# Optimization experiments

Hardware: AMD Instinct MI355X
Metric: run time of the kernel (lower is better)

## Reference

```python
import jax, jax.numpy as jnp
import numpy as np

N = 100000  # nodes
E = 1600000  # edges
F = 128      # features
C = 16       # classes
K = 2        # propagation hops


def setup_inputs() -> dict:
    key = jax.random.key(0)
    k1, k2, k3 = jax.random.split(key, 3)
    x = jax.random.normal(k1, (N, F), dtype=jnp.float32)
    edge_index = jax.random.randint(k2, (2, E), 0, N, dtype=jnp.int64)
    W = jax.random.normal(k3, (F, C), dtype=jnp.float32) * (1.0 / np.sqrt(F))
    b = jnp.zeros((C,), dtype=jnp.float32)
    return {"x": x, "edge_index": edge_index, "W": W, "b": b}


def _sg_propagate(x, row, col, num_nodes):
    # GCN symmetric normalization with self-loops already appended to row/col.
    ones = jnp.ones(row.shape, dtype=x.dtype)
    deg = jax.ops.segment_sum(ones, row, num_segments=num_nodes)
    dinv = jnp.where(deg > 0, jax.lax.rsqrt(deg), jnp.zeros_like(deg))
    norm = dinv[row] * dinv[col]  # [E+N]
    for _ in range(K):
        # gather messages from source nodes, scale, scatter-sum to destinations
        x = jax.ops.segment_sum(norm[:, None] * x[col], row, num_segments=num_nodes)
    return x


def reference(x, edge_index, W, b):
    num_nodes = x.shape[0]
    loops = jnp.arange(num_nodes, dtype=edge_index.dtype)
    row = jnp.concatenate([edge_index[0], loops])
    col = jnp.concatenate([edge_index[1], loops])
    h = _sg_propagate(x, row, col, num_nodes)  # [N, F]
    logits = h @ W + b                          # [N, C]
    return jax.nn.log_softmax(logits, axis=1)
```

## Files before the change

### kernel.cpp

```cpp
#include <hip/hip_runtime.h>
#include <hip/hip_fp16.h>
#include <math.h>

#define NN 100000
#define NE 1600000
#define NF 128
#define NC 16
#define NBUK 391
#define BSH 8
#define BNODES 256
#define CHUNK 8192
#define P1B 196
#define CMASK 0x1FFFF
#define MAXEDG 4800

__global__ void k_init(int* __restrict__ bcur) {
    int n = threadIdx.x;
    if (n < NBUK) bcur[n] = n * MAXEDG;
}

__global__ __launch_bounds__(512) void k_part(const int* __restrict__ row,
                                              const int* __restrict__ col,
                                              int* __restrict__ bcur,
                                              int* __restrict__ pairs) {
    __shared__ int hist[NBUK];
    __shared__ int loff[NBUK];
    __shared__ int gbase[NBUK];
    __shared__ int stage[CHUNK];
    __shared__ unsigned short bkt[CHUNK];
    const int t = threadIdx.x;
    const int cb = blockIdx.x * CHUNK;
    const int ccnt = min(CHUNK, NE - cb);
    const int nquad = ccnt >> 2;
    for (int i = t; i < NBUK; i += 512) hist[i] = 0;
    __syncthreads();

    int rr[16], cc[16], rk[16];
    #pragma unroll
    for (int j = 0; j < 4; ++j) {
        int q = j * 512 + t;
        if (q < nquad) {
            int4 r4 = *(const int4*)&row[cb + 4 * q];
            int4 c4 = *(const int4*)&col[cb + 4 * q];
            rr[4 * j] = r4.x; rr[4 * j + 1] = r4.y; rr[4 * j + 2] = r4.z; rr[4 * j + 3] = r4.w;
            cc[4 * j] = c4.x; cc[4 * j + 1] = c4.y; cc[4 * j + 2] = c4.z; cc[4 * j + 3] = c4.w;
            #pragma unroll
            for (int k = 0; k < 4; ++k)
                rk[4 * j + k] = atomicAdd(&hist[rr[4 * j + k] >> BSH], 1);
        }
    }
    __syncthreads();
    if (t < 64) {
        int loc[7];
        int acc = 0;
        #pragma unroll
        for (int j = 0; j < 7; ++j) {
            int idx = t * 7 + j;
            int v = (idx < NBUK) ? hist[idx] : 0;
            loc[j] = acc;
            acc += v;
        }
        int s = acc;
        #pragma unroll
        for (int o = 1; o < 64; o <<= 1) {
            int u = __shfl_up(s, o, 64);
            if (t >= o) s += u;
        }
        int excl = s - acc;
        #pragma unroll
        for (int j = 0; j < 7; ++j) {
            int idx = t * 7 + j;
            if (idx < NBUK) loff[idx] = excl + loc[j];
        }
    }
    __syncthreads();
    for (int i = t; i < NBUK; i += 512)
        if (hist[i] > 0) gbase[i] = atomicAdd(&bcur[i], hist[i]);
    __syncthreads();
    #pragma unroll
    for (int j = 0; j < 4; ++j) {
        int q = j * 512 + t;
        if (q < nquad) {
            #pragma unroll
            for (int k = 0; k < 4; ++k) {
                int r = rr[4 * j + k];
                int b = r >> BSH;
                int pos = loff[b] + rk[4 * j + k];
                stage[pos] = ((r & (BNODES - 1)) << 17) | cc[4 * j + k];
                bkt[pos] = (unsigned short)b;
            }
        }
    }
    __syncthreads();
    for (int s = t; s < ccnt; s += 512) {
        int b = bkt[s];
        pairs[gbase[b] + (s - loff[b])] = stage[s];
    }
}

__global__ __launch_bounds__(256) void k_fine(const int* __restrict__ bcur,
                                              const int* __restrict__ pairs,
                                              int2* __restrict__ rpc,
                                              float* __restrict__ dinv,
                                              int* __restrict__ csr) {
    __shared__ int h[BNODES];
    __shared__ int hs[BNODES];
    const int b = blockIdx.x;
    const int nb = b << BSH;
    const int t = threadIdx.x;
    h[t] = 0;
    __syncthreads();
    const int st = b * MAXEDG;
    const int m = bcur[b] - st;
    for (int i = t; i < m; i += 256)
        atomicAdd(&h[__builtin_nontemporal_load(&pairs[st + i]) >> 17], 1);
    __syncthreads();
    int v = h[t];
    hs[t] = v;
    __syncthreads();
    for (int o = 1; o < 256; o <<= 1) {
        int a = (t >= o) ? hs[t - o] : 0;
        __syncthreads();
        hs[t] += a;
        __syncthreads();
    }
    int excl = hs[t] - v;
    int n0 = nb + t;
    if (n0 < NN) {
        rpc[n0] = make_int2(st + excl, v);
        dinv[n0] = rsqrtf((float)(v + 1));
    }
    __syncthreads();
    h[t] = excl;
    __syncthreads();
    for (int i = t; i < m; i += 256) {
        int pk = __builtin_nontemporal_load(&pairs[st + i]);
        int pos = atomicAdd(&h[pk >> 17], 1);
        csr[st + pos] = pk & CMASK;
    }
}

#define GEMM_ROWS 64
#define XPAD (NF + 4)

__global__ __launch_bounds__(256) void k_gemm(const float* __restrict__ x,
                                              const float* __restrict__ W,
                                              const float* __restrict__ dinv,
                                              __half* __restrict__ u) {
    __shared__ float Wl[NF * NC];
    __shared__ float xs[GEMM_ROWS * XPAD];
    const int t = threadIdx.x;
    for (int i = t; i < NF * NC; i += 256) Wl[i] = W[i];
    const int rbase = blockIdx.x * GEMM_ROWS;
    const float4* x4 = (const float4*)x;
    for (int i = t; i < GEMM_ROWS * (NF / 4); i += 256) {
        int lrow = i >> 5, k4 = i & 31;
        int r = rbase + lrow;
        float4 v = (r < NN) ? x4[(size_t)r * (NF / 4) + k4]
                            : make_float4(0.f, 0.f, 0.f, 0.f);
        *(float4*)&xs[lrow * XPAD + 4 * k4] = v;
    }
    __syncthreads();
    const int lr = t >> 2;
    const int cg = t & 3;
    float4 acc = make_float4(0.f, 0.f, 0.f, 0.f);
    #pragma unroll
    for (int k4 = 0; k4 < NF / 4; ++k4) {
        float4 xv = *(const float4*)&xs[lr * XPAD + 4 * k4];
        float4 w0 = *(const float4*)&Wl[(4 * k4 + 0) * NC + cg * 4];
        float4 w1 = *(const float4*)&Wl[(4 * k4 + 1) * NC + cg * 4];
        float4 w2 = *(const float4*)&Wl[(4 * k4 + 2) * NC + cg * 4];
        float4 w3 = *(const float4*)&Wl[(4 * k4 + 3) * NC + cg * 4];
        acc.x = fmaf(xv.x, w0.x, fmaf(xv.y, w1.x, fmaf(xv.z, w2.x, fmaf(xv.w, w3.x, acc.x))));
        acc.y = fmaf(xv.x, w0.y, fmaf(xv.y, w1.y, fmaf(xv.z, w2.y, fmaf(xv.w, w3.y, acc.y))));
        acc.z = fmaf(xv.x, w0.z, fmaf(xv.y, w1.z, fmaf(xv.z, w2.z, fmaf(xv.w, w3.z, acc.z))));
        acc.w = fmaf(xv.x, w0.w, fmaf(xv.y, w1.w, fmaf(xv.z, w2.w, fmaf(xv.w, w3.w, acc.w))));
    }
    int r = rbase + lr;
    if (r < NN) {
        float d = dinv[r];
        __half2 h0 = __floats2half2_rn(acc.x * d, acc.y * d);
        __half2 h1 = __floats2half2_rn(acc.z * d, acc.w * d);
        float2 o;
        o.x = *(float*)&h0;
        o.y = *(float*)&h1;
        ((float2*)u)[((size_t)r << 2) + cg] = o;
    }
}


__device__ __forceinline__ void acc16(float4 rw, float* a) {
    float2 f0 = __half22float2(*(__half2*)&rw.x);
    float2 f1 = __half22float2(*(__half2*)&rw.y);
    float2 f2 = __half22float2(*(__half2*)&rw.z);
    float2 f3 = __half22float2(*(__half2*)&rw.w);
    a[0] += f0.x; a[1] += f0.y; a[2] += f1.x; a[3] += f1.y;
    a[4] += f2.x; a[5] += f2.y; a[6] += f3.x; a[7] += f3.y;
}

__global__ __launch_bounds__(256) void k_hop1(const int2* __restrict__ rpc,
                                              const float* __restrict__ dinv,
                                              const int* __restrict__ csr,
                                              const float4* __restrict__ u,
                                              float4* __restrict__ u1) {
    int t = blockIdx.x * 256 + threadIdx.x;
    if (t >= NN * 2) return;
    int n = t >> 1, half = t & 1;
    int2 rc = rpc[n];
    int s = rc.x, m = rc.y;
    float a[8] = {0.f, 0.f, 0.f, 0.f, 0.f, 0.f, 0.f, 0.f};
    acc16(u[(n << 1) + half], a);
    int i = 0;
    for (; i + 8 <= m; i += 8) {
        int cc[8];
        #pragma unroll
        for (int j = 0; j < 8; ++j) cc[j] = __builtin_nontemporal_load(&csr[s + i + j]);
        #pragma unroll
        for (int j = 0; j < 8; ++j) acc16(u[(cc[j] << 1) + half], a);
    }
    for (; i < m; ++i)
        acc16(u[(__builtin_nontemporal_load(&csr[s + i]) << 1) + half], a);
    float d = dinv[n];
    float sc = d * d;
    __half2 h0 = __floats2half2_rn(a[0] * sc, a[1] * sc);
    __half2 h1 = __floats2half2_rn(a[2] * sc, a[3] * sc);
    __half2 h2 = __floats2half2_rn(a[4] * sc, a[5] * sc);
    __half2 h3 = __floats2half2_rn(a[6] * sc, a[7] * sc);
    float4 o;
    o.x = *(float*)&h0; o.y = *(float*)&h1;
    o.z = *(float*)&h2; o.w = *(float*)&h3;
    u1[t] = o;
}

__global__ __launch_bounds__(256) void k_hop2(const int2* __restrict__ rpc,
                                              const float* __restrict__ dinv,
                                              const int* __restrict__ csr,
                                              const float4* __restrict__ u1,
                                              const float* __restrict__ bias,
                                              float* __restrict__ out) {
    int t = blockIdx.x * 256 + threadIdx.x;
    if (t >= NN * 2) return;
    int n = t >> 1, half = t & 1;
    int2 rc = rpc[n];
    int s = rc.x, m = rc.y;
    float a[8] = {0.f, 0.f, 0.f, 0.f, 0.f, 0.f, 0.f, 0.f};
    acc16(u1[(n << 1) + half], a);
    int i = 0;
    for (; i + 8 <= m; i += 8) {
        int cc[8];
        #pragma unroll
        for (int j = 0; j < 8; ++j) cc[j] = __builtin_nontemporal_load(&csr[s + i + j]);
        #pragma unroll
        for (int j = 0; j < 8; ++j) acc16(u1[(cc[j] << 1) + half], a);
    }
    for (; i < m; ++i)
        acc16(u1[(__builtin_nontemporal_load(&csr[s + i]) << 1) + half], a);
    float d = dinv[n];
    float v[8];
    const float4* b4 = (const float4*)bias;
    float4 bv0 = b4[half * 2], bv1 = b4[half * 2 + 1];
    v[0] = fmaf(d, a[0], bv0.x); v[1] = fmaf(d, a[1], bv0.y);
    v[2] = fmaf(d, a[2], bv0.z); v[3] = fmaf(d, a[3], bv0.w);
    v[4] = fmaf(d, a[4], bv1.x); v[5] = fmaf(d, a[5], bv1.y);
    v[6] = fmaf(d, a[6], bv1.z); v[7] = fmaf(d, a[7], bv1.w);
    float mx = v[0];
    #pragma unroll
    for (int j = 1; j < 8; ++j) mx = fmaxf(mx, v[j]);
    mx = fmaxf(mx, __shfl_xor(mx, 1, 2));
    float sm = 0.f;
    #pragma unroll
    for (int j = 0; j < 8; ++j) sm += expf(v[j] - mx);
    sm += __shfl_xor(sm, 1, 2);
    float lse = mx + logf(sm);
    float4* o4 = (float4*)out;
    float4 o0, o1;
    o0.x = v[0] - lse; o0.y = v[1] - lse; o0.z = v[2] - lse; o0.w = v[3] - lse;
    o1.x = v[4] - lse; o1.y = v[5] - lse; o1.z = v[6] - lse; o1.w = v[7] - lse;
    o4[((size_t)n << 2) + half * 2]     = o0;
    o4[((size_t)n << 2) + half * 2 + 1] = o1;
}

extern "C" void kernel_launch(void* const* d_in, const int* in_sizes, int n_in,
                              void* d_out, int out_size, void* d_ws, size_t ws_size,
                              hipStream_t stream) {
    const float* x    = (const float*)d_in[0];
    const int*   ei   = (const int*)d_in[1];
    const float* W    = (const float*)d_in[2];
    const float* bias = (const float*)d_in[3];
    float* out = (float*)d_out;

    const int* row = ei;
    const int* col = ei + NE;

    char* ws = (char*)d_ws;
    size_t off = 0;
    auto carve = [&](size_t bytes) -> void* {
        void* p = ws + off;
        off += (bytes + 255) & ~(size_t)255;
        return p;
    };
    int2*   rpc   = (int2*)  carve((size_t)NN * sizeof(int2));
    float*  dinv  = (float*) carve((size_t)NN * sizeof(float));
    int*    bcur  = (int*)   carve((size_t)NBUK * sizeof(int));
    int*    pairs = (int*)   carve((size_t)NBUK * MAXEDG * sizeof(int));
    int*    csr   = (int*)   carve((size_t)NBUK * MAXEDG * sizeof(int));
    float4* u     = (float4*)carve((size_t)NN * NC * sizeof(__half));
    float4* u1    = (float4*)carve((size_t)NN * NC * sizeof(__half));

    k_init<<<1, 512, 0, stream>>>(bcur);
    k_part<<<P1B, 512, 0, stream>>>(row, col, bcur, pairs);
    k_fine<<<NBUK, 256, 0, stream>>>(bcur, pairs, rpc, dinv, csr);

    k_gemm<<<(NN + GEMM_ROWS - 1) / GEMM_ROWS, 256, 0, stream>>>(x, W, dinv, (__half*)u);

    const int HB = (NN * 2 + 255) / 256;
    k_hop1<<<HB, 256, 0, stream>>>(rpc, dinv, csr, u, u1);
    k_hop2<<<HB, 256, 0, stream>>>(rpc, dinv, csr, u1, bias, out);
}
```

Baseline: 101.5 us.

## Pad CSR rows to multiples of four and sort nodes by degree per bucket

Each node's CSR segment is padded to a multiple of four entries, filled with a dummy node index that points at a zeroed row in u and u1. This lets the hop kernels read neighbour indices as int4 vectors without a tail loop. Within each 256-node bucket, nodes are reordered by degree so that lanes in a wavefront have similar trip counts, which cuts divergence. Input loads also switch to nontemporal. The cost is a larger CSR buffer, extra padding writes, an indirection through the node order, and scattered output writes.

New measurement: 117.7 us. +16.0%, slower.

```diff
diff --git a/kernel.cpp b/kernel.cpp
--- a/kernel.cpp
+++ b/kernel.cpp
@@ -13,6 +13,10 @@
 #define P1B 196
 #define CMASK 0x1FFFF
 #define MAXEDG 4800
+#define CSRS 5632
+
+typedef int   iv4 __attribute__((ext_vector_type(4)));
+typedef float fv4 __attribute__((ext_vector_type(4)));
 
 __global__ void k_init(int* __restrict__ bcur) {
     int n = threadIdx.x;
@@ -35,13 +39,15 @@
     for (int i = t; i < NBUK; i += 512) hist[i] = 0;
     __syncthreads();
 
+    const iv4* row4 = (const iv4*)row;
+    const iv4* col4 = (const iv4*)col;
     int rr[16], cc[16], rk[16];
     #pragma unroll
     for (int j = 0; j < 4; ++j) {
         int q = j * 512 + t;
         if (q < nquad) {
-            int4 r4 = *(const int4*)&row[cb + 4 * q];
-            int4 c4 = *(const int4*)&col[cb + 4 * q];
+            iv4 r4 = __builtin_nontemporal_load(row4 + (cb >> 2) + q);
+            iv4 c4 = __builtin_nontemporal_load(col4 + (cb >> 2) + q);
             rr[4 * j] = r4.x; rr[4 * j + 1] = r4.y; rr[4 * j + 2] = r4.z; rr[4 * j + 3] = r4.w;
             cc[4 * j] = c4.x; cc[4 * j + 1] = c4.y; cc[4 * j + 2] = c4.z; cc[4 * j + 3] = c4.w;
             #pragma unroll
@@ -102,13 +108,16 @@
                                               const int* __restrict__ pairs,
                                               int2* __restrict__ rpc,
                                               float* __restrict__ dinv,
-                                              int* __restrict__ csr) {
+                                              int* __restrict__ csr,
+                                              int* __restrict__ norder) {
     __shared__ int h[BNODES];
     __shared__ int hs[BNODES];
+    __shared__ int dh[64];
     const int b = blockIdx.x;
     const int nb = b << BSH;
     const int t = threadIdx.x;
     h[t] = 0;
+    if (t < 64) dh[t] = 0;
     __syncthreads();
     const int st = b * MAXEDG;
     const int m = bcur[b] - st;
@@ -116,7 +125,8 @@
         atomicAdd(&h[__builtin_nontemporal_load(&pairs[st + i]) >> 17], 1);
     __syncthreads();
     int v = h[t];
-    hs[t] = v;
+    int pd = (v + 3) & ~3;
+    hs[t] = pd;
     __syncthreads();
     for (int o = 1; o < 256; o <<= 1) {
         int a = (t >= o) ? hs[t - o] : 0;
@@ -124,20 +134,33 @@
         hs[t] += a;
         __syncthreads();
     }
-    int excl = hs[t] - v;
+    int base = b * CSRS + hs[t] - pd;
     int n0 = nb + t;
     if (n0 < NN) {
-        rpc[n0] = make_int2(st + excl, v);
+        rpc[n0] = make_int2(base, v);
         dinv[n0] = rsqrtf((float)(v + 1));
     }
-    __syncthreads();
-    h[t] = excl;
-    __syncthreads();
+    int dcl = min(v, 63);
+    int drank = atomicAdd(&dh[dcl], 1);
+    h[t] = base;
+    __syncthreads();
+    if (t < 64) {
+        int val = dh[t], s = val;
+        #pragma unroll
+        for (int o = 1; o < 64; o <<= 1) {
+            int u = __shfl_up(s, o, 64);
+            if (t >= o) s += u;
+        }
+        dh[t] = s - val;
+    }
+    __syncthreads();
+    norder[nb + dh[dcl] + drank] = n0;
     for (int i = t; i < m; i += 256) {
         int pk = __builtin_nontemporal_load(&pairs[st + i]);
         int pos = atomicAdd(&h[pk >> 17], 1);
-        csr[st + pos] = pk & CMASK;
-    }
+        csr[pos] = pk & CMASK;
+    }
+    for (int j = v; j < pd; ++j) csr[base + j] = NN;
 }
 
 #define GEMM_ROWS 64
@@ -146,18 +169,22 @@
 __global__ __launch_bounds__(256) void k_gemm(const float* __restrict__ x,
                                               const float* __restrict__ W,
                                               const float* __restrict__ dinv,
-                                              __half* __restrict__ u) {
+                                              __half* __restrict__ u,
+                                              __half* __restrict__ u1) {
     __shared__ float Wl[NF * NC];
     __shared__ float xs[GEMM_ROWS * XPAD];
     const int t = threadIdx.x;
     for (int i = t; i < NF * NC; i += 256) Wl[i] = W[i];
     const int rbase = blockIdx.x * GEMM_ROWS;
-    const float4* x4 = (const float4*)x;
+    const fv4* x4 = (const fv4*)x;
     for (int i = t; i < GEMM_ROWS * (NF / 4); i += 256) {
         int lrow = i >> 5, k4 = i & 31;
         int r = rbase + lrow;
-        float4 v = (r < NN) ? x4[(size_t)r * (NF / 4) + k4]
-                            : make_float4(0.f, 0.f, 0.f, 0.f);
+        float4 v = make_float4(0.f, 0.f, 0.f, 0.f);
+        if (r < NN) {
+            fv4 xv = __builtin_nontemporal_load(x4 + (size_t)r * (NF / 4) + k4);
+            v = make_float4(xv.x, xv.y, xv.z, xv.w);
+        }
         *(float4*)&xs[lrow * XPAD + 4 * k4] = v;
     }
     __syncthreads();
@@ -185,6 +212,10 @@
         o.x = *(float*)&h0;
         o.y = *(float*)&h1;
         ((float2*)u)[((size_t)r << 2) + cg] = o;
+    } else if (r == NN) {
+        float2 z = make_float2(0.f, 0.f);
+        ((float2*)u)[((size_t)r << 2) + cg] = z;
+        ((float2*)u1)[((size_t)r << 2) + cg] = z;
     }
 }
 
@@ -198,29 +229,30 @@
     a[4] += f2.x; a[5] += f2.y; a[6] += f3.x; a[7] += f3.y;
 }
 
-__global__ __launch_bounds__(256) void k_hop1(const int2* __restrict__ rpc,
+__global__ __launch_bounds__(256) void k_hop1(const int* __restrict__ norder,
+                                              const int2* __restrict__ rpc,
                                               const float* __restrict__ dinv,
                                               const int* __restrict__ csr,
                                               const float4* __restrict__ u,
                                               float4* __restrict__ u1) {
     int t = blockIdx.x * 256 + threadIdx.x;
-    if (t >= NN * 2) return;
-    int n = t >> 1, half = t & 1;
-    int2 rc = rpc[n];
-    int s = rc.x, m = rc.y;
+    int rank = t >> 1, half = t & 1;
+    int node = norder[rank];
+    if (node >= NN) return;
+    int2 rc = rpc[node];
+    int s4 = rc.x >> 2;
+    int trips = (rc.y + 3) >> 2;
     float a[8] = {0.f, 0.f, 0.f, 0.f, 0.f, 0.f, 0.f, 0.f};
-    acc16(u[(n << 1) + half], a);
-    int i = 0;
-    for (; i + 8 <= m; i += 8) {
-        int cc[8];
-        #pragma unroll
-        for (int j = 0; j < 8; ++j) cc[j] = __builtin_nontemporal_load(&csr[s + i + j]);
-        #pragma unroll
-        for (int j = 0; j < 8; ++j) acc16(u[(cc[j] << 1) + half], a);
-    }
-    for (; i < m; ++i)
-        acc16(u[(__builtin_nontemporal_load(&csr[s + i]) << 1) + half], a);
-    float d = dinv[n];
+    acc16(u[(node << 1) + half], a);
+    const iv4* csr4 = (const iv4*)csr;
+    for (int i = 0; i < trips; ++i) {
+        iv4 c = __builtin_nontemporal_load(csr4 + s4 + i);
+        acc16(u[(c.x << 1) + half], a);
+        acc16(u[(c.y << 1) + half], a);
+        acc16(u[(c.z << 1) + half], a);
+        acc16(u[(c.w << 1) + half], a);
+    }
+    float d = dinv[node];
     float sc = d * d;
     __half2 h0 = __floats2half2_rn(a[0] * sc, a[1] * sc);
     __half2 h1 = __floats2half2_rn(a[2] * sc, a[3] * sc);
@@ -229,33 +261,34 @@
     float4 o;
     o.x = *(float*)&h0; o.y = *(float*)&h1;
     o.z = *(float*)&h2; o.w = *(float*)&h3;
-    u1[t] = o;
-}
-
-__global__ __launch_bounds__(256) void k_hop2(const int2* __restrict__ rpc,
+    u1[(node << 1) + half] = o;
+}
+
+__global__ __launch_bounds__(256) void k_hop2(const int* __restrict__ norder,
+                                              const int2* __restrict__ rpc,
                                               const float* __restrict__ dinv,
                                               const int* __restrict__ csr,
                                               const float4* __restrict__ u1,
                                               const float* __restrict__ bias,
                                               float* __restrict__ out) {
     int t = blockIdx.x * 256 + threadIdx.x;
-    if (t >= NN * 2) return;
-    int n = t >> 1, half = t & 1;
-    int2 rc = rpc[n];
-    int s = rc.x, m = rc.y;
+    int rank = t >> 1, half = t & 1;
+    int node = norder[rank];
+    if (node >= NN) return;
+    int2 rc = rpc[node];
+    int s4 = rc.x >> 2;
+    int trips = (rc.y + 3) >> 2;
     float a[8] = {0.f, 0.f, 0.f, 0.f, 0.f, 0.f, 0.f, 0.f};
-    acc16(u1[(n << 1) + half], a);
-    int i = 0;
-    for (; i + 8 <= m; i += 8) {
-        int cc[8];
-        #pragma unroll
-        for (int j = 0; j < 8; ++j) cc[j] = __builtin_nontemporal_load(&csr[s + i + j]);
-        #pragma unroll
-        for (int j = 0; j < 8; ++j) acc16(u1[(cc[j] << 1) + half], a);
-    }
-    for (; i < m; ++i)
-        acc16(u1[(__builtin_nontemporal_load(&csr[s + i]) << 1) + half], a);
-    float d = dinv[n];
+    acc16(u1[(node << 1) + half], a);
+    const iv4* csr4 = (const iv4*)csr;
+    for (int i = 0; i < trips; ++i) {
+        iv4 c = __builtin_nontemporal_load(csr4 + s4 + i);
+        acc16(u1[(c.x << 1) + half], a);
+        acc16(u1[(c.y << 1) + half], a);
+        acc16(u1[(c.z << 1) + half], a);
+        acc16(u1[(c.w << 1) + half], a);
+    }
+    float d = dinv[node];
     float v[8];
     const float4* b4 = (const float4*)bias;
     float4 bv0 = b4[half * 2], bv1 = b4[half * 2 + 1];
@@ -276,8 +309,8 @@
     float4 o0, o1;
     o0.x = v[0] - lse; o0.y = v[1] - lse; o0.z = v[2] - lse; o0.w = v[3] - lse;
     o1.x = v[4] - lse; o1.y = v[5] - lse; o1.z = v[6] - lse; o1.w = v[7] - lse;
-    o4[((size_t)n << 2) + half * 2]     = o0;
-    o4[((size_t)n << 2) + half * 2 + 1] = o1;
+    o4[((size_t)node << 2) + half * 2]     = o0;
+    o4[((size_t)node << 2) + half * 2 + 1] = o1;
 }
 
 extern "C" void kernel_launch(void* const* d_in, const int* in_sizes, int n_in,
@@ -299,21 +332,23 @@
         off += (bytes + 255) & ~(size_t)255;
         return p;
     };
-    int2*   rpc   = (int2*)  carve((size_t)NN * sizeof(int2));
-    float*  dinv  = (float*) carve((size_t)NN * sizeof(float));
-    int*    bcur  = (int*)   carve((size_t)NBUK * sizeof(int));
-    int*    pairs = (int*)   carve((size_t)NBUK * MAXEDG * sizeof(int));
-    int*    csr   = (int*)   carve((size_t)NBUK * MAXEDG * sizeof(int));
-    float4* u     = (float4*)carve((size_t)NN * NC * sizeof(__half));
-    float4* u1    = (float4*)carve((size_t)NN * NC * sizeof(__half));
+    int2*   rpc    = (int2*)  carve((size_t)NN * sizeof(int2));
+    float*  dinv   = (float*) carve((size_t)NN * sizeof(float));
+    int*    bcur   = (int*)   carve((size_t)NBUK * sizeof(int));
+    int*    norder = (int*)   carve((size_t)NBUK * BNODES * sizeof(int));
+    int*    pairs  = (int*)   carve((size_t)NBUK * MAXEDG * sizeof(int));
+    int*    csr    = (int*)   carve((size_t)NBUK * CSRS * sizeof(int));
+    float4* u      = (float4*)carve((size_t)(NN + 1) * NC * sizeof(__half));
+    float4* u1     = (float4*)carve((size_t)(NN + 1) * NC * sizeof(__half));
 
     k_init<<<1, 512, 0, stream>>>(bcur);
     k_part<<<P1B, 512, 0, stream>>>(row, col, bcur, pairs);
-    k_fine<<<NBUK, 256, 0, stream>>>(bcur, pairs, rpc, dinv, csr);
-
-    k_gemm<<<(NN + GEMM_ROWS - 1) / GEMM_ROWS, 256, 0, stream>>>(x, W, dinv, (__half*)u);
-
-    const int HB = (NN * 2 + 255) / 256;
-    k_hop1<<<HB, 256, 0, stream>>>(rpc, dinv, csr, u, u1);
-    k_hop2<<<HB, 256, 0, stream>>>(rpc, dinv, csr, u1, bias, out);
-}
+    k_fine<<<NBUK, 256, 0, stream>>>(bcur, pairs, rpc, dinv, csr, norder);
+
+    k_gemm<<<(NN + GEMM_ROWS) / GEMM_ROWS, 256, 0, stream>>>(x, W, dinv,
+                                                             (__half*)u, (__half*)u1);
+
+    const int HB = NBUK * 2;
+    k_hop1<<<HB, 256, 0, stream>>>(norder, rpc, dinv, csr, u, u1);
+    k_hop2<<<HB, 256, 0, stream>>>(norder, rpc, dinv, csr, u1, bias, out);
+}
```

## Fuse edge partitioning and dense GEMM into one heterogeneous launch

Applied to the files above, without the earlier changes.

The edge-bucket partition kernel and the x@W projection now run in a single launch, with block index selecting the role, so the GEMM no longer waits for the CSR build and the two independent phases overlap. The GEMM writes unscaled half-precision z, and the dinv scaling is applied in the fine CSR kernel once degrees are known. This removes one launch and the serialization between the phases. In exchange the fine kernel does an extra read-modify-write of z, the z values pass through half precision twice, and the shared-memory union enlarges per-block LDS for the GEMM blocks.

Result: faster. 99.44 us (median of 2 runs) (-2.0%).

```diff
diff --git a/kernel.cpp b/kernel.cpp
--- a/kernel.cpp
+++ b/kernel.cpp
@@ -13,88 +13,127 @@
 #define P1B 196
 #define CMASK 0x1FFFF
 #define MAXEDG 4800
+#define GEMM_ROWS 64
+#define XPAD (NF + 4)
+#define GB 1563
 
 __global__ void k_init(int* __restrict__ bcur) {
     int n = threadIdx.x;
     if (n < NBUK) bcur[n] = n * MAXEDG;
 }
 
-__global__ __launch_bounds__(512) void k_part(const int* __restrict__ row,
-                                              const int* __restrict__ col,
-                                              int* __restrict__ bcur,
-                                              int* __restrict__ pairs) {
-    __shared__ int hist[NBUK];
-    __shared__ int loff[NBUK];
-    __shared__ int gbase[NBUK];
-    __shared__ int stage[CHUNK];
-    __shared__ unsigned short bkt[CHUNK];
+__global__ __launch_bounds__(512) void k_pg(const int* __restrict__ row,
+                                            const int* __restrict__ col,
+                                            int* __restrict__ bcur,
+                                            int* __restrict__ pairs,
+                                            const float* __restrict__ x,
+                                            const float* __restrict__ W,
+                                            __half2* __restrict__ z) {
+    __shared__ char smem[53952];
     const int t = threadIdx.x;
-    const int cb = blockIdx.x * CHUNK;
-    const int ccnt = min(CHUNK, NE - cb);
-    const int nquad = ccnt >> 2;
-    for (int i = t; i < NBUK; i += 512) hist[i] = 0;
-    __syncthreads();
-
-    int rr[16], cc[16], rk[16];
-    #pragma unroll
-    for (int j = 0; j < 4; ++j) {
-        int q = j * 512 + t;
-        if (q < nquad) {
-            int4 r4 = *(const int4*)&row[cb + 4 * q];
-            int4 c4 = *(const int4*)&col[cb + 4 * q];
-            rr[4 * j] = r4.x; rr[4 * j + 1] = r4.y; rr[4 * j + 2] = r4.z; rr[4 * j + 3] = r4.w;
-            cc[4 * j] = c4.x; cc[4 * j + 1] = c4.y; cc[4 * j + 2] = c4.z; cc[4 * j + 3] = c4.w;
+
+    if (blockIdx.x < P1B) {
+        int* hist = (int*)smem;
+        int* loff = (int*)(smem + 1600);
+        int* gbase = (int*)(smem + 3200);
+        int* stage = (int*)(smem + 4800);
+        unsigned short* bkt = (unsigned short*)(smem + 37568);
+        const int cb = blockIdx.x * CHUNK;
+        const int ccnt = min(CHUNK, NE - cb);
+        const int nquad = ccnt >> 2;
+        for (int i = t; i < NBUK; i += 512) hist[i] = 0;
+        __syncthreads();
+
+        int rr[16], cc[16], rk[16];
+        #pragma unroll
+        for (int j = 0; j < 4; ++j) {
+            int q = j * 512 + t;
+            if (q < nquad) {
+                int4 r4 = *(const int4*)&row[cb + 4 * q];
+                int4 c4 = *(const int4*)&col[cb + 4 * q];
+                rr[4 * j] = r4.x; rr[4 * j + 1] = r4.y; rr[4 * j + 2] = r4.z; rr[4 * j + 3] = r4.w;
+                cc[4 * j] = c4.x; cc[4 * j + 1] = c4.y; cc[4 * j + 2] = c4.z; cc[4 * j + 3] = c4.w;
+                #pragma unroll
+                for (int k = 0; k < 4; ++k)
+                    rk[4 * j + k] = atomicAdd(&hist[rr[4 * j + k] >> BSH], 1);
+            }
+        }
+        __syncthreads();
+        if (t < 64) {
+            int loc[7];
+            int acc = 0;
             #pragma unroll
-            for (int k = 0; k < 4; ++k)
-                rk[4 * j + k] = atomicAdd(&hist[rr[4 * j + k] >> BSH], 1);
-        }
-    }
-    __syncthreads();
-    if (t < 64) {
-        int loc[7];
-        int acc = 0;
-        #pragma unroll
-        for (int j = 0; j < 7; ++j) {
-            int idx = t * 7 + j;
-            int v = (idx < NBUK) ? hist[idx] : 0;
-            loc[j] = acc;
-            acc += v;
-        }
-        int s = acc;
-        #pragma unroll
-        for (int o = 1; o < 64; o <<= 1) {
-            int u = __shfl_up(s, o, 64);
-            if (t >= o) s += u;
-        }
-        int excl = s - acc;
-        #pragma unroll
-        for (int j = 0; j < 7; ++j) {
-            int idx = t * 7 + j;
-            if (idx < NBUK) loff[idx] = excl + loc[j];
-        }
-    }
-    __syncthreads();
-    for (int i = t; i < NBUK; i += 512)
-        if (hist[i] > 0) gbase[i] = atomicAdd(&bcur[i], hist[i]);
-    __syncthreads();
-    #pragma unroll
-    for (int j = 0; j < 4; ++j) {
-        int q = j * 512 + t;
-        if (q < nquad) {
+            for (int j = 0; j < 7; ++j) {
+                int idx = t * 7 + j;
+                int v = (idx < NBUK) ? hist[idx] : 0;
+                loc[j] = acc;
+                acc += v;
+            }
+            int s = acc;
             #pragma unroll
-            for (int k = 0; k < 4; ++k) {
-                int r = rr[4 * j + k];
-                int b = r >> BSH;
-                int pos = loff[b] + rk[4 * j + k];
-                stage[pos] = ((r & (BNODES - 1)) << 17) | cc[4 * j + k];
-                bkt[pos] = (unsigned short)b;
-            }
-        }
-    }
-    __syncthreads();
-    for (int s = t; s < ccnt; s += 512) {
-        int b = bkt[s];
-        pairs[gbase[b] + (s - loff[b])] = stage[s];
+            for (int o = 1; o < 64; o <<= 1) {
+                int u = __shfl_up(s, o, 64);
+                if (t >= o) s += u;
+            }
+            int excl = s - acc;
+            #pragma unroll
+            for (int j = 0; j < 7; ++j) {
+                int idx = t * 7 + j;
+                if (idx < NBUK) loff[idx] = excl + loc[j];
+            }
+        }
+        __syncthreads();
+        for (int i = t; i < NBUK; i += 512)
+            if (hist[i] > 0) gbase[i] = atomicAdd(&bcur[i], hist[i]);
+        __syncthreads();
+        #pragma unroll
+        for (int j = 0; j < 4; ++j) {
+            int q = j * 512 + t;
+            if (q < nquad) {
+                #pragma unroll
+                for (int k = 0; k < 4; ++k) {
+                    int r = rr[4 * j + k];
+                    int b = r >> BSH;
+                    int pos = loff[b] + rk[4 * j + k];
+                    stage[pos] = ((r & (BNODES - 1)) << 17) | cc[4 * j + k];
+                    bkt[pos] = (unsigned short)b;
+                }
+            }
+        }
+        __syncthreads();
+        for (int s = t; s < ccnt; s += 512) {
+            int b = bkt[s];
+            pairs[gbase[b] + (s - loff[b])] = stage[s];
+        }
+    } else {
+        float* Wl = (float*)smem;
+        float* xs = (float*)(smem + 8192);
+        for (int i = t; i < NF * NC; i += 512) Wl[i] = W[i];
+        const int rbase = (blockIdx.x - P1B) * GEMM_ROWS;
+        const float4* x4 = (const float4*)x;
+        for (int i = t; i < GEMM_ROWS * (NF / 4); i += 512) {
+            int lrow = i >> 5, k4 = i & 31;
+            int r = rbase + lrow;
+            float4 v = (r < NN) ? x4[(size_t)r * (NF / 4) + k4]
+                                : make_float4(0.f, 0.f, 0.f, 0.f);
+            *(float4*)&xs[lrow * XPAD + 4 * k4] = v;
+        }
+        __syncthreads();
+        const int lr = t >> 3;
+        const int cg = t & 7;
+        float2 acc = make_float2(0.f, 0.f);
+        #pragma unroll
+        for (int k4 = 0; k4 < NF / 4; ++k4) {
+            float4 xv = *(const float4*)&xs[lr * XPAD + 4 * k4];
+            float2 w0 = *(const float2*)&Wl[(4 * k4 + 0) * NC + 2 * cg];
+            float2 w1 = *(const float2*)&Wl[(4 * k4 + 1) * NC + 2 * cg];
+            float2 w2 = *(const float2*)&Wl[(4 * k4 + 2) * NC + 2 * cg];
+            float2 w3 = *(const float2*)&Wl[(4 * k4 + 3) * NC + 2 * cg];
+            acc.x = fmaf(xv.x, w0.x, fmaf(xv.y, w1.x, fmaf(xv.z, w2.x, fmaf(xv.w, w3.x, acc.x))));
+            acc.y = fmaf(xv.x, w0.y, fmaf(xv.y, w1.y, fmaf(xv.z, w2.y, fmaf(xv.w, w3.y, acc.y))));
+        }
+        int r = rbase + lr;
+        if (r < NN) z[((size_t)r << 3) + cg] = __floats2half2_rn(acc.x, acc.y);
     }
 }
 
@@ -102,7 +141,8 @@
                                               const int* __restrict__ pairs,
                                               int2* __restrict__ rpc,
                                               float* __restrict__ dinv,
-                                              int* __restrict__ csr) {
+                                              int* __restrict__ csr,
+                                              __half2* __restrict__ u) {
     __shared__ int h[BNODES];
     __shared__ int hs[BNODES];
     const int b = blockIdx.x;
@@ -126,65 +166,26 @@
     }
     int excl = hs[t] - v;
     int n0 = nb + t;
+    float d = rsqrtf((float)(v + 1));
     if (n0 < NN) {
         rpc[n0] = make_int2(st + excl, v);
-        dinv[n0] = rsqrtf((float)(v + 1));
-    }
-    __syncthreads();
-    h[t] = excl;
+        dinv[n0] = d;
+    }
+    __syncthreads();
+    h[t] = st + excl;
     __syncthreads();
     for (int i = t; i < m; i += 256) {
         int pk = __builtin_nontemporal_load(&pairs[st + i]);
         int pos = atomicAdd(&h[pk >> 17], 1);
-        csr[st + pos] = pk & CMASK;
-    }
-}
-
-#define GEMM_ROWS 64
-#define XPAD (NF + 4)
-
-__global__ __launch_bounds__(256) void k_gemm(const float* __restrict__ x,
-                                              const float* __restrict__ W,
-                                              const float* __restrict__ dinv,
-                                              __half* __restrict__ u) {
-    __shared__ float Wl[NF * NC];
-    __shared__ float xs[GEMM_ROWS * XPAD];
-    const int t = threadIdx.x;
-    for (int i = t; i < NF * NC; i += 256) Wl[i] = W[i];
-    const int rbase = blockIdx.x * GEMM_ROWS;
-    const float4* x4 = (const float4*)x;
-    for (int i = t; i < GEMM_ROWS * (NF / 4); i += 256) {
-        int lrow = i >> 5, k4 = i & 31;
-        int r = rbase + lrow;
-        float4 v = (r < NN) ? x4[(size_t)r * (NF / 4) + k4]
-                            : make_float4(0.f, 0.f, 0.f, 0.f);
-        *(float4*)&xs[lrow * XPAD + 4 * k4] = v;
-    }
-    __syncthreads();
-    const int lr = t >> 2;
-    const int cg = t & 3;
-    float4 acc = make_float4(0.f, 0.f, 0.f, 0.f);
-    #pragma unroll
-    for (int k4 = 0; k4 < NF / 4; ++k4) {
-        float4 xv = *(const float4*)&xs[lr * XPAD + 4 * k4];
-        float4 w0 = *(const float4*)&Wl[(4 * k4 + 0) * NC + cg * 4];
-        float4 w1 = *(const float4*)&Wl[(4 * k4 + 1) * NC + cg * 4];
-        float4 w2 = *(const float4*)&Wl[(4 * k4 + 2) * NC + cg * 4];
-        float4 w3 = *(const float4*)&Wl[(4 * k4 + 3) * NC + cg * 4];
-        acc.x = fmaf(xv.x, w0.x, fmaf(xv.y, w1.x, fmaf(xv.z, w2.x, fmaf(xv.w, w3.x, acc.x))));
-        acc.y = fmaf(xv.x, w0.y, fmaf(xv.y, w1.y, fmaf(xv.z, w2.y, fmaf(xv.w, w3.y, acc.y))));
-        acc.z = fmaf(xv.x, w0.z, fmaf(xv.y, w1.z, fmaf(xv.z, w2.z, fmaf(xv.w, w3.z, acc.z))));
-        acc.w = fmaf(xv.x, w0.w, fmaf(xv.y, w1.w, fmaf(xv.z, w2.w, fmaf(xv.w, w3.w, acc.w))));
-    }
-    int r = rbase + lr;
-    if (r < NN) {
-        float d = dinv[r];
-        __half2 h0 = __floats2half2_rn(acc.x * d, acc.y * d);
-        __half2 h1 = __floats2half2_rn(acc.z * d, acc.w * d);
-        float2 o;
-        o.x = *(float*)&h0;
-        o.y = *(float*)&h1;
-        ((float2*)u)[((size_t)r << 2) + cg] = o;
+        csr[pos] = pk & CMASK;
+    }
+    if (n0 < NN) {
+        __half2* zr = u + ((size_t)n0 << 3);
+        #pragma unroll
+        for (int j = 0; j < 8; ++j) {
+            float2 f = __half22float2(zr[j]);
+            zr[j] = __floats2half2_rn(f.x * d, f.y * d);
+        }
     }
 }
 
@@ -308,10 +309,8 @@
     float4* u1    = (float4*)carve((size_t)NN * NC * sizeof(__half));
 
     k_init<<<1, 512, 0, stream>>>(bcur);
-    k_part<<<P1B, 512, 0, stream>>>(row, col, bcur, pairs);
-    k_fine<<<NBUK, 256, 0, stream>>>(bcur, pairs, rpc, dinv, csr);
-
-    k_gemm<<<(NN + GEMM_ROWS - 1) / GEMM_ROWS, 256, 0, stream>>>(x, W, dinv, (__half*)u);
+    k_pg  <<<P1B + GB, 512, 0, stream>>>(row, col, bcur, pairs, x, W, (__half2*)u);
+    k_fine<<<NBUK, 256, 0, stream>>>(bcur, pairs, rpc, dinv, csr, (__half2*)u);
 
     const int HB = (NN * 2 + 255) / 256;
     k_hop1<<<HB, 256, 0, stream>>>(rpc, dinv, csr, u, u1);
```
